# Kernel tuning notes

Measured on AMD Instinct MI355X. Metric: run time of the kernel, lower is better.

Reference implementation:

```python
import jax, jax.numpy as jnp
import numpy as np

N_ATOMS = 20000
N_CG = 1000
N_EDGES = 200000
FEAT = 128
N_RBF = 20
N_CONV = 3
CUTOFF = 5.0
EPS = 1e-15


def swish(x):
    return x * jax.nn.sigmoid(x)


def preprocess_r(r):
    # r: (n, 3) -> dist (n,), unit (n, 3)
    d = jnp.sqrt((r * r + EPS).sum(-1))
    return d, r / d[:, None]


def dist_embed(d, W, b):
    # PainnRadialBasis (learnable_k=False) + Dense + cosine envelope
    k = jnp.arange(1, N_RBF + 1, dtype=d.dtype)
    rbf = jnp.sin(k[None, :] * jnp.pi * d[:, None] / CUTOFF) / d[:, None]
    env = 0.5 * (jnp.cos(jnp.pi * d / CUTOFF) + 1.0) * (d < CUTOFF).astype(d.dtype)
    return (rbf @ W + b) * env[:, None]


def scatter_mean(x, idx, n):
    s = jax.ops.segment_sum(x, idx, num_segments=n)
    cnt = jax.ops.segment_sum(jnp.ones(idx.shape[0], x.dtype), idx, num_segments=n)
    cnt = jnp.maximum(cnt, 1.0)
    return s / cnt.reshape((n,) + (1,) * (x.ndim - 1))


def cg_encoder(z, xyz, cg_xyz, mapping, nbr_list, embed,
               msg_W1, msg_b1, msg_W2, msg_b2, msg_distW, msg_distb,
               upd_U, upd_V, upd_W1, upd_b1, upd_W2, upd_b2,
               cg_W1, cg_b1, cg_W2, cg_b2, cg_distW, cg_distb):
    s = embed[z]                                     # (N, F)
    v = jnp.zeros((s.shape[0], FEAT, 3), s.dtype)    # (N, F, 3)
    src, dst = nbr_list[:, 0], nbr_list[:, 1]
    r_ij = xyz[dst] - xyz[src]
    r_iI = xyz - cg_xyz[mapping]
    d_ij, u_ij = preprocess_r(r_ij)
    d_iI, u_iI = preprocess_r(r_iI)

    S_I = None
    V_I = None
    for i in range(N_CONV):
        # ---- MessageBlock ----
        phi = swish(s @ msg_W1[i] + msg_b1[i]) @ msg_W2[i] + msg_b2[i]          # (N, 3F)
        w_s = dist_embed(d_ij, msg_distW[i], msg_distb[i])                      # (E, 3F)
        inv = (phi[dst] * w_s).reshape(-1, 3, FEAT)                             # (E, 3, F)
        dv_ij = inv[:, 2, :, None] * u_ij[:, None, :] + inv[:, 0, :, None] * v[dst]
        s = s + jax.ops.segment_sum(inv[:, 1, :], src, num_segments=N_ATOMS)
        v = v + jax.ops.segment_sum(dv_ij, src, num_segments=N_ATOMS)
        # ---- UpdateBlock ----
        u_v = jnp.einsum('nfd,fg->ngd', v, upd_U[i])
        v_v = jnp.einsum('nfd,fg->ngd', v, upd_V[i])
        v_v_norm = jnp.sqrt((v_v * v_v + EPS).sum(-1))                          # (N, F)
        stack = swish(jnp.concatenate([s, v_v_norm], -1) @ upd_W1[i] + upd_b1[i]) @ upd_W2[i] + upd_b2[i]
        a_vv = stack[:, :FEAT, None]
        a_sv = stack[:, FEAT:2 * FEAT]
        a_ss = stack[:, 2 * FEAT:]
        v = v + u_v * a_vv
        s = s + (u_v * v_v).sum(-1) * a_sv + a_ss
        # ---- init CG features after first conv ----
        if i == 0:
            S_I = scatter_mean(s, mapping, N_CG)
            V_I = jnp.zeros((N_CG, FEAT, 3), s.dtype)
        # ---- ContractiveMessageBlock ----
        phi_cg = swish(s @ cg_W1[i] + cg_b1[i]) @ cg_W2[i] + cg_b2[i]           # (N, 3F)
        w_cg = dist_embed(d_iI, cg_distW[i], cg_distb[i])
        inv_cg = (phi_cg * w_cg).reshape(-1, 3, FEAT)
        dv_iI = inv_cg[:, 2, :, None] * u_iI[:, None, :] + inv_cg[:, 0, :, None] * v
        S_I = S_I + scatter_mean(inv_cg[:, 1, :], mapping, N_CG)
        V_I = V_I + scatter_mean(dv_iI, mapping, N_CG)
    return S_I


def setup_inputs() -> dict:
    key = jax.random.key(0)
    ks = jax.random.split(key, 20)
    p = lambda i, shape: jax.random.normal(ks[i], shape, jnp.float32) * 0.05
    return {
        'z': jax.random.randint(ks[0], (N_ATOMS,), 1, 100),
        'xyz': jax.random.normal(ks[1], (N_ATOMS, 3), jnp.float32),
        'cg_xyz': jax.random.normal(ks[2], (N_CG, 3), jnp.float32),
        'mapping': jax.random.randint(ks[3], (N_ATOMS,), 0, N_CG),
        'nbr_list': jax.random.randint(ks[4], (N_EDGES, 2), 0, N_ATOMS),
        'embed': p(5, (100, FEAT)).at[0].set(0.0),  # padding_idx=0
        'msg_W1': p(6, (N_CONV, FEAT, FEAT)), 'msg_b1': jnp.zeros((N_CONV, FEAT)),
        'msg_W2': p(7, (N_CONV, FEAT, 3 * FEAT)), 'msg_b2': jnp.zeros((N_CONV, 3 * FEAT)),
        'msg_distW': p(8, (N_CONV, N_RBF, 3 * FEAT)), 'msg_distb': jnp.zeros((N_CONV, 3 * FEAT)),
        'upd_U': p(9, (N_CONV, FEAT, FEAT)), 'upd_V': p(10, (N_CONV, FEAT, FEAT)),
        'upd_W1': p(11, (N_CONV, 2 * FEAT, FEAT)), 'upd_b1': jnp.zeros((N_CONV, FEAT)),
        'upd_W2': p(12, (N_CONV, FEAT, 3 * FEAT)), 'upd_b2': jnp.zeros((N_CONV, 3 * FEAT)),
        'cg_W1': p(13, (N_CONV, FEAT, FEAT)), 'cg_b1': jnp.zeros((N_CONV, FEAT)),
        'cg_W2': p(14, (N_CONV, FEAT, 3 * FEAT)), 'cg_b2': jnp.zeros((N_CONV, 3 * FEAT)),
        'cg_distW': p(15, (N_CONV, N_RBF, 3 * FEAT)), 'cg_distb': jnp.zeros((N_CONV, 3 * FEAT)),
    }


def reference(z, xyz, cg_xyz, mapping, nbr_list, embed,
              msg_W1, msg_b1, msg_W2, msg_b2, msg_distW, msg_distb,
              upd_U, upd_V, upd_W1, upd_b1, upd_W2, upd_b2,
              cg_W1, cg_b1, cg_W2, cg_b2, cg_distW, cg_distb):
    return cg_encoder(z, xyz, cg_xyz, mapping, nbr_list, embed,
                      msg_W1, msg_b1, msg_W2, msg_b2, msg_distW, msg_distb,
                      upd_U, upd_V, upd_W1, upd_b1, upd_W2, upd_b2,
                      cg_W1, cg_b1, cg_W2, cg_b2, cg_distW, cg_distb)
```

## Files before the change

kernel.cpp:

```cpp
#include <hip/hip_runtime.h>
#include <math.h>

#define N_ATOMS 20000
#define N_CG    1000
#define N_EDGES 200000
#define FEAT    128
#define NRBF    20
#define NCONV   3
#define CUTOFF  5.0f
#define PLANE   (N_ATOMS * FEAT)
#define PI_F    3.14159265358979323846f
#define LDH     130

#define PACK_PER_CONV 212992

typedef __attribute__((ext_vector_type(8))) short bf16x8;
typedef __attribute__((ext_vector_type(4))) float f32x4;

__device__ __forceinline__ void split2(float x, ushort& h, ushort& l)
{
    unsigned u  = __float_as_uint(x);
    unsigned hb = (u + 0x7FFFu + ((u >> 16) & 1u)) & 0xFFFF0000u;
    float    hf = __uint_as_float(hb);
    float    lf = x - hf;
    unsigned ul = __float_as_uint(lf);
    h = (ushort)(hb >> 16);
    l = (ushort)((ul + 0x7FFFu + ((ul >> 16) & 1u)) >> 16);
}

__device__ __forceinline__ void splitv8(const float* hv, bf16x8& ah, bf16x8& al)
{
#pragma unroll
    for (int j = 0; j < 8; ++j) {
        ushort h, l;
        split2(hv[j], h, l);
        ah[j] = (short)h; al[j] = (short)l;
    }
}

#define MFMA3(ACC, AH_, AL_, BH_, BL_)                                              \
    ACC = __builtin_amdgcn_mfma_f32_16x16x32_bf16(AH_, BH_, ACC, 0, 0, 0);          \
    ACC = __builtin_amdgcn_mfma_f32_16x16x32_bf16(AH_, BL_, ACC, 0, 0, 0);          \
    ACC = __builtin_amdgcn_mfma_f32_16x16x32_bf16(AL_, BH_, ACC, 0, 0, 0);

template<int K1, int N2>
__global__ __launch_bounds__(256)
void mlp_fused(const ushort* __restrict__ AH, const ushort* __restrict__ AL,
               const ushort* __restrict__ B1h, const ushort* __restrict__ B1l,
               const float* __restrict__ b1,
               const ushort* __restrict__ B2h, const ushort* __restrict__ B2l,
               const float* __restrict__ b2, int bcol0,
               float* __restrict__ C)
{
    __shared__ float Hs[32 * LDH];
    const int tid  = threadIdx.x;
    const int lane = tid & 63;
    const int w    = tid >> 6;
    const int wm   = w & 1, wn = w >> 1;
    const int m0   = blockIdx.x * 32;
    const int l15  = lane & 15;
    const int koff = (lane >> 4) * 8;
    const int rowb = wm * 16;
    const int q4   = (lane >> 4) * 4;

    f32x4 acc1[4];
#pragma unroll
    for (int j = 0; j < 4; ++j) acc1[j] = (f32x4){0.f, 0.f, 0.f, 0.f};
    for (int k0 = 0; k0 < K1; k0 += 32) {
        size_t aa = (size_t)(m0 + rowb + l15) * K1 + k0 + koff;
        bf16x8 ah = *reinterpret_cast<const bf16x8*>(AH + aa);
        bf16x8 al = *reinterpret_cast<const bf16x8*>(AL + aa);
#pragma unroll
        for (int nf = 0; nf < 4; ++nf) {
            size_t ba = (size_t)(wn * 64 + nf * 16 + l15) * K1 + k0 + koff;
            bf16x8 bh = *reinterpret_cast<const bf16x8*>(B1h + ba);
            bf16x8 bl = *reinterpret_cast<const bf16x8*>(B1l + ba);
            MFMA3(acc1[nf], ah, al, bh, bl);
        }
    }
#pragma unroll
    for (int nf = 0; nf < 4; ++nf) {
        int col = wn * 64 + nf * 16 + l15;
        float bv = b1[col];
#pragma unroll
        for (int r = 0; r < 4; ++r) {
            float x = acc1[nf][r] + bv;
            x = x / (1.f + __expf(-x));
            Hs[(rowb + q4 + r) * LDH + col] = x;
        }
    }
    __syncthreads();

    constexpr int NF2  = N2 / 32;
    constexpr int WCOL = N2 / 2;
    f32x4 acc2[NF2];
#pragma unroll
    for (int j = 0; j < NF2; ++j) acc2[j] = (f32x4){0.f, 0.f, 0.f, 0.f};
    for (int k0 = 0; k0 < 128; k0 += 32) {
        const float* hp = &Hs[(rowb + l15) * LDH + k0 + koff];
        float hv[8];
#pragma unroll
        for (int j = 0; j < 4; ++j) hv[j] = hp[j];
#pragma unroll
        for (int j = 0; j < 4; ++j) hv[4 + j] = hp[4 + j];
        bf16x8 ah, al;
        splitv8(hv, ah, al);
#pragma unroll
        for (int nf = 0; nf < NF2; ++nf) {
            size_t ba = (size_t)(wn * WCOL + nf * 16 + l15) * 128 + k0 + koff;
            bf16x8 bh = *reinterpret_cast<const bf16x8*>(B2h + ba);
            bf16x8 bl = *reinterpret_cast<const bf16x8*>(B2l + ba);
            MFMA3(acc2[nf], ah, al, bh, bl);
        }
    }
#pragma unroll
    for (int nf = 0; nf < NF2; ++nf) {
        int col = wn * WCOL + nf * 16 + l15;
        float bv = b2 ? b2[bcol0 + col] : 0.f;
#pragma unroll
        for (int r = 0; r < 4; ++r) {
            int row = m0 + rowb + q4 + r;
            C[(size_t)row * N2 + col] = acc2[nf][r] + bv;
        }
    }
}

__global__ __launch_bounds__(256)
void gemm_vnorm(const ushort* __restrict__ vHp, const ushort* __restrict__ vLp,
                const ushort* __restrict__ Bh, const ushort* __restrict__ Bl,
                float* __restrict__ vv,
                ushort* __restrict__ CcatH, ushort* __restrict__ CcatL)
{
    const int tid  = threadIdx.x;
    const int lane = tid & 63;
    const int w    = tid >> 6;
    const int wm   = w & 1, wn = w >> 1;
    const int m0   = blockIdx.x * 32;
    const int l15  = lane & 15;
    const int koff = (lane >> 4) * 8;
    const int rowb = wm * 16;
    const int q4   = (lane >> 4) * 4;

    f32x4 acc[3][4];
#pragma unroll
    for (int d = 0; d < 3; ++d)
#pragma unroll
        for (int j = 0; j < 4; ++j) acc[d][j] = (f32x4){0.f, 0.f, 0.f, 0.f};

    for (int k0 = 0; k0 < 128; k0 += 32) {
        bf16x8 ah[3], al[3];
#pragma unroll
        for (int d = 0; d < 3; ++d) {
            size_t aa = (size_t)d * PLANE + (size_t)(m0 + rowb + l15) * 128 + k0 + koff;
            ah[d] = *reinterpret_cast<const bf16x8*>(vHp + aa);
            al[d] = *reinterpret_cast<const bf16x8*>(vLp + aa);
        }
#pragma unroll
        for (int nf = 0; nf < 4; ++nf) {
            size_t ba = (size_t)(wn * 64 + nf * 16 + l15) * 128 + k0 + koff;
            bf16x8 bh = *reinterpret_cast<const bf16x8*>(Bh + ba);
            bf16x8 bl = *reinterpret_cast<const bf16x8*>(Bl + ba);
#pragma unroll
            for (int d = 0; d < 3; ++d) {
                MFMA3(acc[d][nf], ah[d], al[d], bh, bl);
            }
        }
    }
#pragma unroll
    for (int nf = 0; nf < 4; ++nf) {
        int col = wn * 64 + nf * 16 + l15;
#pragma unroll
        for (int r = 0; r < 4; ++r) {
            int row = m0 + rowb + q4 + r;
            int idx = row * FEAT + col;
            float x = acc[0][nf][r], y = acc[1][nf][r], z = acc[2][nf][r];
            vv[idx] = x; vv[PLANE + idx] = y; vv[2 * PLANE + idx] = z;
            float nrm = sqrtf(x * x + y * y + z * z + 3e-15f);
            ushort h, l;
            split2(nrm, h, l);
            CcatH[(size_t)row * 256 + 128 + col] = h;
            CcatL[(size_t)row * 256 + 128 + col] = l;
        }
    }
}

__global__ __launch_bounds__(256)
void gemm_u_update(const ushort* __restrict__ vHp, const ushort* __restrict__ vLp,
                   const ushort* __restrict__ Bh, const ushort* __restrict__ Bl,
                   const float* __restrict__ vv, const float* __restrict__ stack,
                   float* __restrict__ s, float* __restrict__ v,
                   ushort* __restrict__ sH, ushort* __restrict__ sL)
{
    const int tid  = threadIdx.x;
    const int lane = tid & 63;
    const int w    = tid >> 6;
    const int wm   = w & 1, wn = w >> 1;
    const int m0   = blockIdx.x * 32;
    const int l15  = lane & 15;
    const int koff = (lane >> 4) * 8;
    const int rowb = wm * 16;
    const int q4   = (lane >> 4) * 4;

    f32x4 acc[3][4];
#pragma unroll
    for (int d = 0; d < 3; ++d)
#pragma unroll
        for (int j = 0; j < 4; ++j) acc[d][j] = (f32x4){0.f, 0.f, 0.f, 0.f};

    for (int k0 = 0; k0 < 128; k0 += 32) {
        bf16x8 ah[3], al[3];
#pragma unroll
        for (int d = 0; d < 3; ++d) {
            size_t aa = (size_t)d * PLANE + (size_t)(m0 + rowb + l15) * 128 + k0 + koff;
            ah[d] = *reinterpret_cast<const bf16x8*>(vHp + aa);
            al[d] = *reinterpret_cast<const bf16x8*>(vLp + aa);
        }
#pragma unroll
        for (int nf = 0; nf < 4; ++nf) {
            size_t ba = (size_t)(wn * 64 + nf * 16 + l15) * 128 + k0 + koff;
            bf16x8 bh = *reinterpret_cast<const bf16x8*>(Bh + ba);
            bf16x8 bl = *reinterpret_cast<const bf16x8*>(Bl + ba);
#pragma unroll
            for (int d = 0; d < 3; ++d) {
                MFMA3(acc[d][nf], ah[d], al[d], bh, bl);
            }
        }
    }
    ushort* vHo = const_cast<ushort*>(vHp);
    ushort* vLo = const_cast<ushort*>(vLp);
#pragma unroll
    for (int nf = 0; nf < 4; ++nf) {
        int col = wn * 64 + nf * 16 + l15;
#pragma unroll
        for (int r = 0; r < 4; ++r) {
            int row = m0 + rowb + q4 + r;
            int idx = row * FEAT + col;
            const float* st = stack + (size_t)row * 384 + col;
            float avv = st[0], asv = st[128], ass = st[256];
            float u0 = acc[0][nf][r], u1 = acc[1][nf][r], u2 = acc[2][nf][r];
            float w0 = vv[idx], w1 = vv[PLANE + idx], w2 = vv[2 * PLANE + idx];
            float dot = u0 * w0 + u1 * w1 + u2 * w2;
            float n0 = v[idx]             + u0 * avv;
            float n1 = v[PLANE + idx]     + u1 * avv;
            float n2 = v[2 * PLANE + idx] + u2 * avv;
            v[idx] = n0; v[PLANE + idx] = n1; v[2 * PLANE + idx] = n2;
            ushort h, l;
            split2(n0, h, l); vHo[idx] = h;             vLo[idx] = l;
            split2(n1, h, l); vHo[PLANE + idx] = h;     vLo[PLANE + idx] = l;
            split2(n2, h, l); vHo[2 * PLANE + idx] = h; vLo[2 * PLANE + idx] = l;
            float ns = s[idx] + dot * asv + ass;
            s[idx] = ns;
            split2(ns, h, l); sH[idx] = h; sL[idx] = l;
        }
    }
}

__global__ void k_pack_all(const float* __restrict__ msg_W1, const float* __restrict__ msg_W2,
                           const float* __restrict__ upd_V,  const float* __restrict__ upd_W1,
                           const float* __restrict__ upd_W2, const float* __restrict__ upd_U,
                           const float* __restrict__ cg_W1,  const float* __restrict__ cg_W2,
                           ushort* __restrict__ Bh, ushort* __restrict__ Bl)
{
    const int wid = blockIdx.y, conv = blockIdx.z;
    const float* W; int K, N, ldw, col0; size_t off;
    switch (wid) {
        case 0: W = msg_W1 + (size_t)conv * 16384; K = 128; N = 128; ldw = 128; col0 = 0;   off = 0;      break;
        case 1: W = msg_W2 + (size_t)conv * 49152; K = 128; N = 384; ldw = 384; col0 = 0;   off = 16384;  break;
        case 2: W = upd_V  + (size_t)conv * 16384; K = 128; N = 128; ldw = 128; col0 = 0;   off = 65536;  break;
        case 3: W = upd_W1 + (size_t)conv * 32768; K = 256; N = 128; ldw = 128; col0 = 0;   off = 81920;  break;
        case 4: W = upd_W2 + (size_t)conv * 49152; K = 128; N = 384; ldw = 384; col0 = 0;   off = 114688; break;
        case 5: W = upd_U  + (size_t)conv * 16384; K = 128; N = 128; ldw = 128; col0 = 0;   off = 163840; break;
        case 6: W = cg_W1  + (size_t)conv * 16384; K = 128; N = 128; ldw = 128; col0 = 0;   off = 180224; break;
        default:W = cg_W2  + (size_t)conv * 49152; K = 128; N = 128; ldw = 384; col0 = 128; off = 196608; break;
    }
    off += (size_t)conv * PACK_PER_CONV;
    int idx = blockIdx.x * 256 + threadIdx.x;
    if (idx >= K * N) return;
    int k = idx & (K - 1);
    int n = idx >> ((K == 256) ? 8 : 7);
    ushort h, l;
    split2(W[(size_t)k * ldw + col0 + n], h, l);
    Bh[off + (size_t)n * K + k] = h;
    Bl[off + (size_t)n * K + k] = l;
}

__global__ void k_s_init(const int* __restrict__ z, const float* __restrict__ embed,
                         float* __restrict__ s, ushort* __restrict__ sH, ushort* __restrict__ sL)
{
    int idx = blockIdx.x * blockDim.x + threadIdx.x;
    if (idx >= PLANE) return;
    int n = idx >> 7, g = idx & 127;
    float e = embed[z[n] * FEAT + g];
    s[idx] = e;
    ushort h, l;
    split2(e, h, l);
    sH[idx] = h; sL[idx] = l;
}

__global__ void k_atom_geo(const int* __restrict__ mapping,
                           const float* __restrict__ xyz, const float* __restrict__ cg_xyz,
                           float* __restrict__ rbf_a, float* __restrict__ env_a,
                           float* __restrict__ cnt)
{
    int n = blockIdx.x * blockDim.x + threadIdx.x;
    if (n >= N_ATOMS) return;
    int m = mapping[n];
    float dx = xyz[n * 3 + 0] - cg_xyz[m * 3 + 0];
    float dy = xyz[n * 3 + 1] - cg_xyz[m * 3 + 1];
    float dz = xyz[n * 3 + 2] - cg_xyz[m * 3 + 2];
    float d = sqrtf(dx * dx + dy * dy + dz * dz + 3e-15f);
    float env = (d < CUTOFF) ? 0.5f * (cosf(PI_F * d / CUTOFF) + 1.f) : 0.f;
    env_a[n] = env;
    float s = env / d;
#pragma unroll
    for (int k = 0; k < NRBF; ++k)
        rbf_a[n * NRBF + k] = sinf((k + 1) * PI_F * d / CUTOFF) * s;
    atomicAdd(&cnt[m], 1.f);
}

__global__ void k_deg(const int* __restrict__ nbr, int* __restrict__ deg)
{
    int e = blockIdx.x * blockDim.x + threadIdx.x;
    if (e < N_EDGES) atomicAdd(&deg[nbr[2 * e]], 1);
}

__global__ __launch_bounds__(1024)
void k_scan(const int* __restrict__ deg, int* __restrict__ rowptr)
{
    __shared__ int sh[1024];
    const int chunk = (N_ATOMS + 1023) / 1024;
    int t = threadIdx.x;
    int base = t * chunk;
    int sum = 0;
    for (int i = 0; i < chunk; ++i) {
        int idx = base + i;
        if (idx < N_ATOMS) sum += deg[idx];
    }
    sh[t] = sum;
    __syncthreads();
    for (int off = 1; off < 1024; off <<= 1) {
        int val = (t >= off) ? sh[t - off] : 0;
        __syncthreads();
        sh[t] += val;
        __syncthreads();
    }
    int run = (t == 0) ? 0 : sh[t - 1];
    for (int i = 0; i < chunk; ++i) {
        int idx = base + i;
        if (idx < N_ATOMS) { rowptr[idx] = run; run += deg[idx]; }
    }
}

__global__ void k_fill(const int* __restrict__ nbr, const float* __restrict__ xyz,
                       const int* __restrict__ rowptr, int* __restrict__ cursor,
                       int* __restrict__ rec_dst, float4* __restrict__ rec_u4,
                       float* __restrict__ rec_rbf)
{
    int e = blockIdx.x * blockDim.x + threadIdx.x;
    if (e >= N_EDGES) return;
    int src = nbr[2 * e], dst = nbr[2 * e + 1];
    int pos = atomicAdd(&cursor[src], 1);
    int q = rowptr[src] + pos;
    float dx = xyz[dst * 3 + 0] - xyz[src * 3 + 0];
    float dy = xyz[dst * 3 + 1] - xyz[src * 3 + 1];
    float dz = xyz[dst * 3 + 2] - xyz[src * 3 + 2];
    float d = sqrtf(dx * dx + dy * dy + dz * dz + 3e-15f);
    float env = (d < CUTOFF) ? 0.5f * (cosf(PI_F * d / CUTOFF) + 1.f) : 0.f;
    rec_dst[q] = dst;
    rec_u4[q] = make_float4(dx / d, dy / d, dz / d, env);
    float sc = env / d;
#pragma unroll
    for (int k = 0; k < NRBF; ++k)
        rec_rbf[(size_t)q * NRBF + k] = sinf((k + 1) * PI_F * d / CUTOFF) * sc;
}

__global__ __launch_bounds__(512)
void k_edge_seg(const int* __restrict__ rowptr, const int* __restrict__ deg,
                const int* __restrict__ rec_dst, const float4* __restrict__ rec_u4,
                const float* __restrict__ rec_rbf,
                const float* __restrict__ phi,
                const float* __restrict__ v_in, float* __restrict__ v_out,
                float* __restrict__ s,
                ushort* __restrict__ vH, ushort* __restrict__ vL,
                ushort* __restrict__ CcatH, ushort* __restrict__ CcatL,
                const float* __restrict__ distW, const float* __restrict__ distb)
{
    __shared__ f32x4 shW[21 * 128];
    const int tid = threadIdx.x;
    for (int i = tid; i < 21 * 128; i += 512) {
        int k = i >> 7, f = i & 127;
        const float* src = (k < 20) ? (distW + k * 384) : distb;
        shW[i] = (f32x4){src[f], src[128 + f], src[256 + f], 0.f};
    }
    __syncthreads();
    const int slot = tid >> 7;
    const int f    = tid & 127;
    const int a    = blockIdx.x;
    const int beg  = rowptr[a];
    const int end  = beg + deg[a];
    float s_acc = 0.f, vx = 0.f, vy = 0.f, vz = 0.f;

    for (int p = beg + slot; p < end; p += 4) {
        float4 u4 = rec_u4[p];
        int dst = rec_dst[p];
        if (u4.w == 0.f) continue;
        const float* ph = phi + (size_t)dst * 384 + f;
        float p0 = ph[0], p1 = ph[128], p2 = ph[256];
        int di = dst * FEAT + f;
        float vdx = v_in[di], vdy = v_in[PLANE + di], vdz = v_in[2 * PLANE + di];
        const float4* rbp = reinterpret_cast<const float4*>(rec_rbf + (size_t)p * NRBF);
        float4 r0 = rbp[0], r1 = rbp[1], r2 = rbp[2], r3 = rbp[3], r4 = rbp[4];
        const float rr[21] = {r0.x, r0.y, r0.z, r0.w, r1.x, r1.y, r1.z, r1.w,
                              r2.x, r2.y, r2.z, r2.w, r3.x, r3.y, r3.z, r3.w,
                              r4.x, r4.y, r4.z, r4.w, u4.w};
        float w0 = 0.f, w1 = 0.f, w2 = 0.f;
#pragma unroll
        for (int k = 0; k < 21; ++k) {
            f32x4 wk = shW[(k << 7) + f];
            w0 += rr[k] * wk.x;
            w1 += rr[k] * wk.y;
            w2 += rr[k] * wk.z;
        }
        float i0 = p0 * w0, i1 = p1 * w1, i2 = p2 * w2;
        vx += i2 * u4.x + i0 * vdx;
        vy += i2 * u4.y + i0 * vdy;
        vz += i2 * u4.z + i0 * vdz;
        s_acc += i1;
    }

    __syncthreads();
    f32x4* red = shW;
    red[tid] = (f32x4){s_acc, vx, vy, vz};
    __syncthreads();
    if (slot == 0) {
        f32x4 t = red[f] + red[128 + f] + red[256 + f] + red[384 + f];
        int si = a * FEAT + f;
        float ns = s[si] + t.x;
        s[si] = ns;
        float nx = v_in[si]             + t.y;
        float ny = v_in[PLANE + si]     + t.z;
        float nz = v_in[2 * PLANE + si] + t.w;
        v_out[si] = nx; v_out[PLANE + si] = ny; v_out[2 * PLANE + si] = nz;
        ushort h, l;
        split2(nx, h, l); vH[si] = h;             vL[si] = l;
        split2(ny, h, l); vH[PLANE + si] = h;     vL[PLANE + si] = l;
        split2(nz, h, l); vH[2 * PLANE + si] = h; vL[2 * PLANE + si] = l;
        split2(ns, h, l);
        CcatH[(size_t)a * 256 + f] = h;
        CcatL[(size_t)a * 256 + f] = l;
    }
}

__global__ __launch_bounds__(128)
void k_cg_msg(const int* __restrict__ mapping, const float* __restrict__ phi_mid,
              const float* __restrict__ rbf_a, const float* __restrict__ env_a,
              const float* __restrict__ distW, const float* __restrict__ distb,
              const float* __restrict__ s_add, float* __restrict__ S_acc)
{
    int n = blockIdx.x;
    float env = env_a[n];
    int f = threadIdx.x;
    if (env == 0.f && s_add == nullptr) return;
    float val = s_add ? s_add[n * FEAT + f] : 0.f;
    if (env != 0.f) {
        __shared__ float sh_rbf[NRBF];
        if (f < NRBF) sh_rbf[f] = rbf_a[n * NRBF + f];
        __syncthreads();
        float w1 = 0.f;
#pragma unroll
        for (int k = 0; k < NRBF; ++k)
            w1 += sh_rbf[k] * distW[k * 384 + 128 + f];
        w1 += distb[128 + f] * env;
        val += phi_mid[n * FEAT + f] * w1;
    }
    atomicAdd(&S_acc[mapping[n] * FEAT + f], val);
}

__global__ void k_finalize(const float* __restrict__ S_acc, const float* __restrict__ cnt,
                           float* __restrict__ out, int add)
{
    int idx = blockIdx.x * blockDim.x + threadIdx.x;
    if (idx >= N_CG * FEAT) return;
    float val = S_acc[idx] / fmaxf(cnt[idx >> 7], 1.f);
    if (add) out[idx] += val;
    else     out[idx] = val;
}

extern "C" void kernel_launch(void* const* d_in, const int* in_sizes, int n_in,
                              void* d_out, int out_size, void* d_ws, size_t ws_size,
                              hipStream_t stream)
{
    const int*   z        = (const int*)d_in[0];
    const float* xyz      = (const float*)d_in[1];
    const float* cg_xyz   = (const float*)d_in[2];
    const int*   mapping  = (const int*)d_in[3];
    const int*   nbr      = (const int*)d_in[4];
    const float* embed    = (const float*)d_in[5];
    const float* msg_W1   = (const float*)d_in[6];
    const float* msg_b1   = (const float*)d_in[7];
    const float* msg_W2   = (const float*)d_in[8];
    const float* msg_b2   = (const float*)d_in[9];
    const float* msg_dW   = (const float*)d_in[10];
    const float* msg_db   = (const float*)d_in[11];
    const float* upd_U    = (const float*)d_in[12];
    const float* upd_V    = (const float*)d_in[13];
    const float* upd_W1   = (const float*)d_in[14];
    const float* upd_b1   = (const float*)d_in[15];
    const float* upd_W2   = (const float*)d_in[16];
    const float* upd_b2   = (const float*)d_in[17];
    const float* cg_W1    = (const float*)d_in[18];
    const float* cg_b1    = (const float*)d_in[19];
    const float* cg_W2    = (const float*)d_in[20];
    const float* cg_b2    = (const float*)d_in[21];
    const float* cg_dW    = (const float*)d_in[22];
    const float* cg_db    = (const float*)d_in[23];
    float* out = (float*)d_out;

    float* ws = (float*)d_ws;
    size_t o = 0;
    float* s      = ws + o; o += PLANE;
    float* vA     = ws + o; o += 3 * PLANE;
    float* vB     = ws + o; o += 3 * PLANE;
    float* uv     = ws + o; o += PLANE;
    float* phi    = ws + o; o += (size_t)N_ATOMS * 384;
    float* Cpk    = ws + o; o += (size_t)N_ATOMS * 256;
    float* spk    = ws + o; o += PLANE;
    float* vpk    = ws + o; o += 3 * PLANE;
    float4* rec_u4 = (float4*)(ws + o); o += (size_t)N_EDGES * 4;
    float* rec_rbf = ws + o; o += (size_t)N_EDGES * NRBF;
    int*   rec_dst = (int*)(ws + o); o += N_EDGES;
    float* rbf_a  = ws + o; o += (size_t)N_ATOMS * NRBF;
    float* env_a  = ws + o; o += N_ATOMS;
    float* cnt    = ws + o; o += N_CG;
    float* S_acc  = ws + o; o += N_CG * FEAT;
    int*   deg    = (int*)(ws + o); o += N_ATOMS;
    int*   rowptr = (int*)(ws + o); o += N_ATOMS;
    int*   cursor = (int*)(ws + o); o += N_ATOMS;
    ushort* packH = (ushort*)(ws + o); o += (size_t)NCONV * PACK_PER_CONV / 2;
    ushort* packL = (ushort*)(ws + o); o += (size_t)NCONV * PACK_PER_CONV / 2;

    ushort* CcatH = (ushort*)Cpk; ushort* CcatL = CcatH + (size_t)N_ATOMS * 256;
    ushort* sH = (ushort*)spk;  ushort* sL = sH + PLANE;
    ushort* vH = (ushort*)vpk;  ushort* vL = vH + 3 * PLANE;

    hipMemsetAsync(vA, 0, sizeof(float) * 3 * PLANE, stream);
    hipMemsetAsync(cnt, 0, sizeof(float) * N_CG, stream);
    hipMemsetAsync(deg, 0, sizeof(int) * N_ATOMS, stream);
    hipMemsetAsync(cursor, 0, sizeof(int) * N_ATOMS, stream);
    k_pack_all<<<dim3(192, 8, 3), 256, 0, stream>>>(msg_W1, msg_W2, upd_V, upd_W1,
                                                    upd_W2, upd_U, cg_W1, cg_W2,
                                                    packH, packL);
    k_s_init<<<(PLANE + 255) / 256, 256, 0, stream>>>(z, embed, s, sH, sL);
    k_atom_geo<<<(N_ATOMS + 255) / 256, 256, 0, stream>>>(mapping, xyz, cg_xyz,
                                                          rbf_a, env_a, cnt);
    k_deg<<<(N_EDGES + 255) / 256, 256, 0, stream>>>(nbr, deg);
    k_scan<<<1, 1024, 0, stream>>>(deg, rowptr);
    k_fill<<<(N_EDGES + 255) / 256, 256, 0, stream>>>(nbr, xyz, rowptr, cursor,
                                                      rec_dst, rec_u4, rec_rbf);

    float* v_cur = vA;
    float* v_nxt = vB;

    for (int i = 0; i < NCONV; ++i) {
        const float* mb1 = msg_b1 + (size_t)i * FEAT;
        const float* mb2 = msg_b2 + (size_t)i * 384;
        const float* mdW = msg_dW + (size_t)i * NRBF * 384;
        const float* mdb = msg_db + (size_t)i * 384;
        const float* ub1 = upd_b1 + (size_t)i * FEAT;
        const float* ub2 = upd_b2 + (size_t)i * 384;
        const float* cb1 = cg_b1  + (size_t)i * FEAT;
        const float* cb2 = cg_b2  + (size_t)i * 384;
        const float* cdW = cg_dW  + (size_t)i * NRBF * 384;
        const float* cdb = cg_db  + (size_t)i * 384;
        const size_t pb  = (size_t)i * PACK_PER_CONV;

        mlp_fused<128, 384><<<625, 256, 0, stream>>>(
            sH, sL, packH + pb + 0, packL + pb + 0, mb1,
            packH + pb + 16384, packL + pb + 16384, mb2, 0, phi);
        k_edge_seg<<<N_ATOMS, 512, 0, stream>>>(rowptr, deg, rec_dst, rec_u4,
                                                rec_rbf, phi, v_cur, v_nxt, s,
                                                vH, vL, CcatH, CcatL, mdW, mdb);
        float* vv = v_cur;

        gemm_vnorm<<<625, 256, 0, stream>>>(vH, vL, packH + pb + 65536,
                                            packL + pb + 65536, vv, CcatH, CcatL);
        mlp_fused<256, 384><<<625, 256, 0, stream>>>(
            CcatH, CcatL, packH + pb + 81920, packL + pb + 81920, ub1,
            packH + pb + 114688, packL + pb + 114688, ub2, 0, phi);
        gemm_u_update<<<625, 256, 0, stream>>>(vH, vL, packH + pb + 163840,
                                               packL + pb + 163840, vv, phi,
                                               s, v_nxt, sH, sL);

        mlp_fused<128, 128><<<625, 256, 0, stream>>>(
            sH, sL, packH + pb + 180224, packL + pb + 180224, cb1,
            packH + pb + 196608, packL + pb + 196608, cb2, 128, uv);
        hipMemsetAsync(S_acc, 0, sizeof(float) * N_CG * FEAT, stream);
        k_cg_msg<<<N_ATOMS, 128, 0, stream>>>(mapping, uv, rbf_a, env_a, cdW, cdb,
                                              (i == 0) ? s : nullptr, S_acc);
        k_finalize<<<(N_CG * FEAT + 255) / 256, 256, 0, stream>>>(S_acc, cnt, out,
                                                                  i == 0 ? 0 : 1);

        float* tmp = v_nxt;
        v_nxt = v_cur;
        v_cur = tmp;
    }
}
```

Before: 1.462 ms.

## Hold edge distance-embedding weights in registers with persistent atom-loop blocks

The edge segment kernel now launches a fixed 2500 blocks that stride over atoms, instead of one block per atom. Each thread loads its 63 distance-embedding weights once into registers rather than having every block refill a shared-memory weight table. This removes the per-atom shared-memory fill and a barrier, and replaces shared-memory reads with register operands in the inner loop. It raises register pressure, with launch bounds asking for 4 blocks per unit, and with fewer blocks there is less latency hiding and worse balance across uneven atom degrees.

```diff
diff --git a/kernel.cpp b/kernel.cpp
--- a/kernel.cpp
+++ b/kernel.cpp
@@ -374,7 +374,8 @@
         rec_rbf[(size_t)q * NRBF + k] = sinf((k + 1) * PI_F * d / CUTOFF) * sc;
 }
 
-__global__ __launch_bounds__(512)
+#define EDGE_BLOCKS 2500
+__global__ __launch_bounds__(512, 4)
 void k_edge_seg(const int* __restrict__ rowptr, const int* __restrict__ deg,
                 const int* __restrict__ rec_dst, const float4* __restrict__ rec_u4,
                 const float* __restrict__ rec_rbf,
@@ -385,69 +386,74 @@
                 ushort* __restrict__ CcatH, ushort* __restrict__ CcatL,
                 const float* __restrict__ distW, const float* __restrict__ distb)
 {
-    __shared__ f32x4 shW[21 * 128];
-    const int tid = threadIdx.x;
-    for (int i = tid; i < 21 * 128; i += 512) {
-        int k = i >> 7, f = i & 127;
-        const float* src = (k < 20) ? (distW + k * 384) : distb;
-        shW[i] = (f32x4){src[f], src[128 + f], src[256 + f], 0.f};
-    }
-    __syncthreads();
+    __shared__ f32x4 red[512];
+    const int tid  = threadIdx.x;
     const int slot = tid >> 7;
     const int f    = tid & 127;
-    const int a    = blockIdx.x;
-    const int beg  = rowptr[a];
-    const int end  = beg + deg[a];
-    float s_acc = 0.f, vx = 0.f, vy = 0.f, vz = 0.f;
-
-    for (int p = beg + slot; p < end; p += 4) {
-        float4 u4 = rec_u4[p];
-        int dst = rec_dst[p];
-        if (u4.w == 0.f) continue;
-        const float* ph = phi + (size_t)dst * 384 + f;
-        float p0 = ph[0], p1 = ph[128], p2 = ph[256];
-        int di = dst * FEAT + f;
-        float vdx = v_in[di], vdy = v_in[PLANE + di], vdz = v_in[2 * PLANE + di];
-        const float4* rbp = reinterpret_cast<const float4*>(rec_rbf + (size_t)p * NRBF);
-        float4 r0 = rbp[0], r1 = rbp[1], r2 = rbp[2], r3 = rbp[3], r4 = rbp[4];
-        const float rr[21] = {r0.x, r0.y, r0.z, r0.w, r1.x, r1.y, r1.z, r1.w,
-                              r2.x, r2.y, r2.z, r2.w, r3.x, r3.y, r3.z, r3.w,
-                              r4.x, r4.y, r4.z, r4.w, u4.w};
-        float w0 = 0.f, w1 = 0.f, w2 = 0.f;
-#pragma unroll
-        for (int k = 0; k < 21; ++k) {
-            f32x4 wk = shW[(k << 7) + f];
-            w0 += rr[k] * wk.x;
-            w1 += rr[k] * wk.y;
-            w2 += rr[k] * wk.z;
-        }
-        float i0 = p0 * w0, i1 = p1 * w1, i2 = p2 * w2;
-        vx += i2 * u4.x + i0 * vdx;
-        vy += i2 * u4.y + i0 * vdy;
-        vz += i2 * u4.z + i0 * vdz;
-        s_acc += i1;
-    }
-
-    __syncthreads();
-    f32x4* red = shW;
-    red[tid] = (f32x4){s_acc, vx, vy, vz};
-    __syncthreads();
-    if (slot == 0) {
-        f32x4 t = red[f] + red[128 + f] + red[256 + f] + red[384 + f];
-        int si = a * FEAT + f;
-        float ns = s[si] + t.x;
-        s[si] = ns;
-        float nx = v_in[si]             + t.y;
-        float ny = v_in[PLANE + si]     + t.z;
-        float nz = v_in[2 * PLANE + si] + t.w;
-        v_out[si] = nx; v_out[PLANE + si] = ny; v_out[2 * PLANE + si] = nz;
-        ushort h, l;
-        split2(nx, h, l); vH[si] = h;             vL[si] = l;
-        split2(ny, h, l); vH[PLANE + si] = h;     vL[PLANE + si] = l;
-        split2(nz, h, l); vH[2 * PLANE + si] = h; vL[2 * PLANE + si] = l;
-        split2(ns, h, l);
-        CcatH[(size_t)a * 256 + f] = h;
-        CcatL[(size_t)a * 256 + f] = l;
+
+    float wx[21], wy[21], wz[21];
+#pragma unroll
+    for (int k = 0; k < NRBF; ++k) {
+        wx[k] = distW[k * 384 + f];
+        wy[k] = distW[k * 384 + 128 + f];
+        wz[k] = distW[k * 384 + 256 + f];
+    }
+    wx[20] = distb[f];
+    wy[20] = distb[128 + f];
+    wz[20] = distb[256 + f];
+
+    for (int a = blockIdx.x; a < N_ATOMS; a += EDGE_BLOCKS) {
+        const int beg = rowptr[a];
+        const int end = beg + deg[a];
+        float s_acc = 0.f, vx = 0.f, vy = 0.f, vz = 0.f;
+
+        for (int p = beg + slot; p < end; p += 4) {
+            float4 u4 = rec_u4[p];
+            int dst = rec_dst[p];
+            if (u4.w == 0.f) continue;
+            const float* ph = phi + (size_t)dst * 384 + f;
+            float p0 = ph[0], p1 = ph[128], p2 = ph[256];
+            int di = dst * FEAT + f;
+            float vdx = v_in[di], vdy = v_in[PLANE + di], vdz = v_in[2 * PLANE + di];
+            const float4* rbp = reinterpret_cast<const float4*>(rec_rbf + (size_t)p * NRBF);
+            float4 r0 = rbp[0], r1 = rbp[1], r2 = rbp[2], r3 = rbp[3], r4 = rbp[4];
+            const float rr[21] = {r0.x, r0.y, r0.z, r0.w, r1.x, r1.y, r1.z, r1.w,
+                                  r2.x, r2.y, r2.z, r2.w, r3.x, r3.y, r3.z, r3.w,
+                                  r4.x, r4.y, r4.z, r4.w, u4.w};
+            float w0 = 0.f, w1 = 0.f, w2 = 0.f;
+#pragma unroll
+            for (int k = 0; k < 21; ++k) {
+                w0 += rr[k] * wx[k];
+                w1 += rr[k] * wy[k];
+                w2 += rr[k] * wz[k];
+            }
+            float i0 = p0 * w0, i1 = p1 * w1, i2 = p2 * w2;
+            vx += i2 * u4.x + i0 * vdx;
+            vy += i2 * u4.y + i0 * vdy;
+            vz += i2 * u4.z + i0 * vdz;
+            s_acc += i1;
+        }
+
+        __syncthreads();
+        red[tid] = (f32x4){s_acc, vx, vy, vz};
+        __syncthreads();
+        if (slot == 0) {
+            f32x4 t = red[f] + red[128 + f] + red[256 + f] + red[384 + f];
+            int si = a * FEAT + f;
+            float ns = s[si] + t.x;
+            s[si] = ns;
+            float nx = v_in[si]             + t.y;
+            float ny = v_in[PLANE + si]     + t.z;
+            float nz = v_in[2 * PLANE + si] + t.w;
+            v_out[si] = nx; v_out[PLANE + si] = ny; v_out[2 * PLANE + si] = nz;
+            ushort h, l;
+            split2(nx, h, l); vH[si] = h;             vL[si] = l;
+            split2(ny, h, l); vH[PLANE + si] = h;     vL[PLANE + si] = l;
+            split2(nz, h, l); vH[2 * PLANE + si] = h; vL[2 * PLANE + si] = l;
+            split2(ns, h, l);
+            CcatH[(size_t)a * 256 + f] = h;
+            CcatL[(size_t)a * 256 + f] = l;
+        }
     }
 }
 
@@ -577,9 +583,9 @@
         mlp_fused<128, 384><<<625, 256, 0, stream>>>(
             sH, sL, packH + pb + 0, packL + pb + 0, mb1,
             packH + pb + 16384, packL + pb + 16384, mb2, 0, phi);
-        k_edge_seg<<<N_ATOMS, 512, 0, stream>>>(rowptr, deg, rec_dst, rec_u4,
-                                                rec_rbf, phi, v_cur, v_nxt, s,
-                                                vH, vL, CcatH, CcatL, mdW, mdb);
+        k_edge_seg<<<EDGE_BLOCKS, 512, 0, stream>>>(rowptr, deg, rec_dst, rec_u4,
+                                                    rec_rbf, phi, v_cur, v_nxt, s,
+                                                    vH, vL, CcatH, CcatL, mdW, mdb);
         float* vv = v_cur;
 
         gemm_vnorm<<<625, 256, 0, stream>>>(vH, vL, packH + pb + 65536,
```

Result: faster. 1.375 ms (-6.0%).
